# Kernel tuning notes

Hardware: AMD Instinct MI355X
Metric: run time of the kernel (lower is better)

The kernel has to match this reference:

```python
import jax, jax.numpy as jnp
import numpy as np

NUM_ITEMS = 1000000   # catalog size; id == NUM_ITEMS is the padding item
B, S = 512, 200       # batch, sequence length
M, SUB = 8, 32        # pq_m bytes per item, sub-embedding size (embedding_size = M*SUB = 256)
NUM_CENTROIDS = 256   # uint8 code range


def setup_inputs() -> dict:
    key = jax.random.key(0)
    k1, k2, k3 = jax.random.split(key, 3)
    input_ids = jax.random.randint(k1, (B, S), 0, NUM_ITEMS + 1, dtype=jnp.int64)
    # item_codes: PQ code table, one byte (0..255) per item per code-byte
    item_codes = jax.random.randint(k2, (NUM_ITEMS + 1, M), 0, NUM_CENTROIDS, dtype=jnp.int32)
    # centroids: per-byte codebooks, uniform init as in tf.random_uniform_initializer()
    centroids = jax.random.uniform(k3, (M, NUM_CENTROIDS, SUB), dtype=jnp.float32)
    return {"input_ids": input_ids, "item_codes": item_codes, "centroids": centroids}


def reference(input_ids, item_codes, centroids):
    # codes[b,s,i] = PQ byte i of item input_ids[b,s]
    codes = item_codes[input_ids]                                  # [B, S, M] int32
    byte_idx = jnp.arange(codes.shape[-1])[None, None, :]          # [1, 1, M]
    # gather centroid vector per (byte, code): centroids[i, codes[b,s,i], :]
    sub_emb = centroids[byte_idx, codes]                           # [B, S, M, SUB]
    b, s = input_ids.shape
    return sub_emb.reshape(b, s, codes.shape[-1] * centroids.shape[-1])  # [B, S, M*SUB]
```

## Files before the change

kernel.cpp:

```cpp
#include <hip/hip_runtime.h>
#include <hip/hip_bf16.h>


#define M_BYTES 8
#define SUB_DIM 32
#define EMB     (M_BYTES * SUB_DIM)

__global__ __launch_bounds__(256) void ItemCodeLayer_30253749633338_kernel(
    const int*   __restrict__ ids,
    const int*   __restrict__ codes,
    const float* __restrict__ cent,
    float*       __restrict__ out,
    int n_tokens)
{
    const int tid = blockIdx.x * blockDim.x + threadIdx.x;
    const int token = tid >> 6;
    if (token >= n_tokens) return;
    const int l = tid & 63;
    const int m = l >> 3;
    const int j = (l & 7) * 4;

    const int id   = ids[token];
    const int code = codes[(size_t)id * M_BYTES + m];

    const float4* src = reinterpret_cast<const float4*>(
        cent + ((size_t)(m * 256 + code) * SUB_DIM + j));
    float4 v = *src;

    float4* dst = reinterpret_cast<float4*>(
        out + ((size_t)token * EMB + m * SUB_DIM + j));
    *dst = v;
}

extern "C" void kernel_launch(void* const* d_in, const int* in_sizes, int n_in,
                              void* d_out, int out_size, void* d_ws, size_t ws_size,
                              hipStream_t stream) {
    const int*   ids   = (const int*)  d_in[0];
    const int*   codes = (const int*)  d_in[1];
    const float* cent  = (const float*)d_in[2];
    float*       out   = (float*)      d_out;

    const int n_tokens = in_sizes[0];
    const long long total_threads = (long long)n_tokens * 64;
    const int block = 256;
    const int grid  = (int)((total_threads + block - 1) / block);

    hipLaunchKernelGGL(ItemCodeLayer_30253749633338_kernel,
                       dim3(grid), dim3(block), 0, stream,
                       ids, codes, cent, out, n_tokens);
}
```

Before: 147.1 us.

## Stage PQ codes in shared memory and process many tokens per block

New measurement: 131.1 us. -10.9%, faster.

```diff
diff --git a/kernel.cpp b/kernel.cpp
--- a/kernel.cpp
+++ b/kernel.cpp
@@ -5,31 +5,59 @@
 #define M_BYTES 8
 #define SUB_DIM 32
 #define EMB     (M_BYTES * SUB_DIM)
+#define TOK_PER_BLOCK 64
+#define BLOCK 256
 
-__global__ __launch_bounds__(256) void ItemCodeLayer_30253749633338_kernel(
+__global__ __launch_bounds__(BLOCK) void ItemCodeLayer_30253749633338_kernel(
     const int*   __restrict__ ids,
     const int*   __restrict__ codes,
     const float* __restrict__ cent,
     float*       __restrict__ out,
     int n_tokens)
 {
-    const int tid = blockIdx.x * blockDim.x + threadIdx.x;
-    const int token = tid >> 6;
-    if (token >= n_tokens) return;
-    const int l = tid & 63;
-    const int m = l >> 3;
-    const int j = (l & 7) * 4;
+    __shared__ int s_codes[TOK_PER_BLOCK * M_BYTES];
 
-    const int id   = ids[token];
-    const int code = codes[(size_t)id * M_BYTES + m];
+    const int tid  = threadIdx.x;
+    const int base = blockIdx.x * TOK_PER_BLOCK;
 
-    const float4* src = reinterpret_cast<const float4*>(
-        cent + ((size_t)(m * 256 + code) * SUB_DIM + j));
-    float4 v = *src;
+    const int t0 = tid >> 3;
+    const int m  = tid & 7;
+    const int t1 = t0 + 32;
 
-    float4* dst = reinterpret_cast<float4*>(
-        out + ((size_t)token * EMB + m * SUB_DIM + j));
-    *dst = v;
+    int id0 = (base + t0 < n_tokens) ? ids[base + t0] : 0;
+    int id1 = (base + t1 < n_tokens) ? ids[base + t1] : 0;
+
+    int c0 = codes[(size_t)id0 * M_BYTES + m];
+    int c1 = codes[(size_t)id1 * M_BYTES + m];
+    s_codes[t0 * M_BYTES + m] = c0;
+    s_codes[t1 * M_BYTES + m] = c1;
+    __syncthreads();
+
+    const int wave = tid >> 6;
+    const int l    = tid & 63;
+    const int lm   = l >> 3;
+    const int lj   = (l & 7) * 4;
+
+    #pragma unroll
+    for (int it = 0; it < 16; it += 4) {
+        int   tk[4];
+        float4 v[4];
+        #pragma unroll
+        for (int u = 0; u < 4; ++u) {
+            tk[u] = (it + u) * 4 + wave;
+            int code = s_codes[tk[u] * M_BYTES + lm];
+            v[u] = *reinterpret_cast<const float4*>(
+                cent + ((size_t)(lm * 256 + code) * SUB_DIM + lj));
+        }
+        #pragma unroll
+        for (int u = 0; u < 4; ++u) {
+            int t = base + tk[u];
+            if (t < n_tokens) {
+                *reinterpret_cast<float4*>(
+                    out + ((size_t)t * EMB + lm * SUB_DIM + lj)) = v[u];
+            }
+        }
+    }
 }
 
 extern "C" void kernel_launch(void* const* d_in, const int* in_sizes, int n_in,
@@ -41,11 +69,9 @@
     float*       out   = (float*)      d_out;
 
     const int n_tokens = in_sizes[0];
-    const long long total_threads = (long long)n_tokens * 64;
-    const int block = 256;
-    const int grid  = (int)((total_threads + block - 1) / block);
+    const int grid = (n_tokens + TOK_PER_BLOCK - 1) / TOK_PER_BLOCK;
 
     hipLaunchKernelGGL(ItemCodeLayer_30253749633338_kernel,
-                       dim3(grid), dim3(block), 0, stream,
+                       dim3(grid), dim3(BLOCK), 0, stream,
                        ids, codes, cent, out, n_tokens);
 }
```
